# Kernel tuning notes

Hardware: AMD Instinct MI355X
Metric: run time of the kernel (lower is better)

Reference implementation:

```python
import jax, jax.numpy as jnp
import numpy as np

N, E = 50000, 800000          # nodes, edges
F_IN, H, C = 32, 64, 7        # input feats, hidden, classes
EPS = 1e-5                    # BatchNorm eps


def setup_inputs() -> dict:
    key = jax.random.key(0)
    ks = jax.random.split(key, 16)
    inp = {
        "x": jax.random.normal(ks[0], (N, F_IN), jnp.float32),
        "edge_index": jax.random.randint(ks[1], (2, E), 0, N),
        "edge_attr": jax.random.uniform(ks[2], (E, 1), jnp.float32),
    }

    def conv_params(k, cin, cout, i):
        k1, k2 = jax.random.split(k)
        s = 1.0 / np.sqrt(cin)
        inp[f"W{i}"] = jax.random.uniform(k1, (2, cin, cout), jnp.float32, -s, s)  # spline kernel weights
        inp[f"R{i}"] = jax.random.uniform(k2, (cin, cout), jnp.float32, -s, s)     # root weight
        inp[f"B{i}"] = jnp.zeros((cout,), jnp.float32)

    conv_params(ks[3], F_IN, H, 0)
    conv_params(ks[4], H, H, 1)
    conv_params(ks[5], H, C, 2)
    for i in range(2):  # BatchNorm (eval mode: running stats)
        inp[f"G{i}"] = jnp.ones((H,), jnp.float32)
        inp[f"BE{i}"] = jnp.zeros((H,), jnp.float32)
        inp[f"RM{i}"] = 0.1 * jax.random.normal(ks[6 + 2 * i], (H,), jnp.float32)
        inp[f"RV{i}"] = jax.random.uniform(ks[7 + 2 * i], (H,), jnp.float32, 0.5, 1.5)
    return inp


def spline_conv(x, src, dst, u, W, R, B):
    # dim=1, kernel_size=2, degree=1 open B-spline:
    # basis = (1-u, u) with weight indices (0, 1) for u in [0,1).
    basis = jnp.stack([1.0 - u, u], axis=1)               # [E, 2]
    msg = jnp.einsum('ec,ek,kco->eo', x[src], basis, W)    # gather + basis-weighted linear
    agg = jax.ops.segment_sum(msg, dst, num_segments=N)    # scatter-add
    deg = jax.ops.segment_sum(jnp.ones((src.shape[0],), x.dtype), dst, num_segments=N)
    agg = agg / jnp.maximum(deg, 1.0)[:, None]             # aggr='mean' (default)
    return agg + x @ R + B                                 # root weight + bias


def batch_norm(x, g, b, rm, rv):
    return (x - rm) * jax.lax.rsqrt(rv + EPS) * g + b


def reference(x, edge_index, edge_attr,
              W0, R0, B0, W1, R1, B1, W2, R2, B2,
              G0, BE0, RM0, RV0, G1, BE1, RM1, RV1):
    src, dst = edge_index[0], edge_index[1]
    u = edge_attr[:, 0]
    h = spline_conv(x, src, dst, u, W0, R0, B0)
    h = jax.nn.elu(batch_norm(h, G0, BE0, RM0, RV0))
    h = spline_conv(h, src, dst, u, W1, R1, B1)
    h = jax.nn.elu(batch_norm(h, G1, BE1, RM1, RV1))
    h = spline_conv(h, src, dst, u, W2, R2, B2)
    return jax.nn.log_softmax(h, axis=1)
```

## Files before the change

kernel.cpp:

```cpp
#include <hip/hip_runtime.h>
#include <hip/hip_fp16.h>
#include <math.h>

#define NN 50000
#define NE 800000
#define EPSV 1e-5f
#define BSHIFT 7
#define BSIZE 128
#define NB 391
#define CAP 3840

typedef _Float16 h2f   __attribute__((ext_vector_type(2)));
typedef _Float16 f16x8 __attribute__((ext_vector_type(8)));
typedef float    f32x4 __attribute__((ext_vector_type(4)));

__global__ __launch_bounds__(64) void prep_all_kernel(
        const float* __restrict__ W0, const float* __restrict__ R0,
        const float* __restrict__ W1, const float* __restrict__ R1,
        const float* __restrict__ W2, const float* __restrict__ R2,
        const float* __restrict__ B0, const float* __restrict__ B1,
        const float* __restrict__ G0, const float* __restrict__ BE0,
        const float* __restrict__ RM0, const float* __restrict__ RV0,
        const float* __restrict__ G1, const float* __restrict__ BE1,
        const float* __restrict__ RM1, const float* __restrict__ RV1,
        __half* __restrict__ Bf0, __half* __restrict__ Bf1, __half* __restrict__ Bf7,
        float* __restrict__ bn0, float* __restrict__ bn1,
        int* __restrict__ bcursor) {
    int lane = threadIdx.x;
    int bid = blockIdx.x;
    int c = lane & 15;
    int kbase = ((lane >> 4) << 3);
    _Float16 vals[8];
    if (bid < 12) {
        int ks = bid >> 2, nt = bid & 3;
        int n = nt * 16 + c;
#pragma unroll
        for (int j = 0; j < 8; ++j) {
            int kg = ks * 32 + kbase + j;
            float v = (kg < 64) ? W0[(kg & 1) * 2048 + (kg >> 1) * 64 + n]
                                : R0[(kg - 64) * 64 + n];
            vals[j] = (_Float16)v;
        }
        *reinterpret_cast<f16x8*>(Bf0 + ((size_t)(bid * 64 + lane)) * 8) =
            *reinterpret_cast<f16x8*>(vals);
    } else if (bid < 36) {
        int t = bid - 12;
        int ks = t >> 2, nt = t & 3;
        int n = nt * 16 + c;
#pragma unroll
        for (int j = 0; j < 8; ++j) {
            int kg = ks * 32 + kbase + j;
            float v = (kg < 128) ? W1[(kg & 1) * 4096 + (kg >> 1) * 64 + n]
                                 : R1[(kg - 128) * 64 + n];
            vals[j] = (_Float16)v;
        }
        *reinterpret_cast<f16x8*>(Bf1 + ((size_t)(t * 64 + lane)) * 8) =
            *reinterpret_cast<f16x8*>(vals);
    } else if (bid < 40) {
        int ksnt = bid - 36;
        int ks = ksnt >> 1, nt = ksnt & 1;
#pragma unroll
        for (int j = 0; j < 8; ++j) {
            int k = ks * 32 + kbase + j;
            float v = 0.f;
            if (nt == 0) {
                if (c < 7)                 v = W2[k * 7 + c];
                else if (c >= 8 && c < 15) v = W2[448 + k * 7 + (c - 8)];
            } else {
                if (c < 7)                 v = R2[k * 7 + c];
            }
            vals[j] = (_Float16)v;
        }
        *reinterpret_cast<f16x8*>(Bf7 + ((size_t)(ksnt * 64 + lane)) * 8) =
            *reinterpret_cast<f16x8*>(vals);
    } else if (bid == 40) {
        float s = G0[lane] * rsqrtf(RV0[lane] + EPSV);
        bn0[lane] = s;
        bn0[64 + lane] = B0[lane] * s + BE0[lane] - RM0[lane] * s;
    } else if (bid == 41) {
        float s = G1[lane] * rsqrtf(RV1[lane] + EPSV);
        bn1[lane] = s;
        bn1[64 + lane] = B1[lane] * s + BE1[lane] - RM1[lane] * s;
    } else {
        int b = (bid - 42) * 64 + lane;
        if (b < NB) bcursor[b] = b * CAP;
    }
}

__global__ __launch_bounds__(256) void binB_xh_kernel(
        const int* __restrict__ src, const int* __restrict__ dst,
        const float* __restrict__ attr, int* __restrict__ bcursor,
        unsigned* __restrict__ es1su, unsigned char* __restrict__ es1dl, int E,
        const float* __restrict__ x, __half* __restrict__ xh) {
    __shared__ int hist[NB];
    __shared__ int base[NB];
    if (blockIdx.x >= NB) {
        int t = (blockIdx.x - NB) * 256 + threadIdx.x;
        size_t idx = (size_t)t * 8;
        if (idx < (size_t)NN * 32) {
            float4 f0 = *reinterpret_cast<const float4*>(x + idx);
            float4 f1 = *reinterpret_cast<const float4*>(x + idx + 4);
            _Float16 v[8] = {(_Float16)f0.x, (_Float16)f0.y, (_Float16)f0.z, (_Float16)f0.w,
                             (_Float16)f1.x, (_Float16)f1.y, (_Float16)f1.z, (_Float16)f1.w};
            *reinterpret_cast<f16x8*>(xh + idx) = *reinterpret_cast<f16x8*>(v);
        }
        return;
    }
    for (int i = threadIdx.x; i < NB; i += blockDim.x) hist[i] = 0;
    __syncthreads();
    const int chunk = (E + NB - 1) / NB;
    int e0 = blockIdx.x * chunk;
    int e1 = e0 + chunk; if (e1 > E) e1 = E;
    unsigned su[8]; unsigned char dlv[8]; short bv[8];
#pragma unroll
    for (int j = 0; j < 8; ++j) {
        int e = e0 + threadIdx.x + j * 256;
        if (e < e1) {
            int d = dst[e];
            int b = d >> BSHIFT;
            __half uh = __float2half_rn(attr[e]);
            su[j]  = ((unsigned)src[e] << 16) | (unsigned)__half_as_ushort(uh);
            dlv[j] = (unsigned char)(d & (BSIZE - 1));
            bv[j]  = (short)b;
            atomicAdd(&hist[b], 1);
        }
    }
    __syncthreads();
    for (int i = threadIdx.x; i < NB; i += blockDim.x) {
        int cnt = hist[i];
        base[i] = cnt ? atomicAdd(&bcursor[i], cnt) : 0;
        hist[i] = 0;
    }
    __syncthreads();
#pragma unroll
    for (int j = 0; j < 8; ++j) {
        int e = e0 + threadIdx.x + j * 256;
        if (e < e1) {
            int b = bv[j];
            int slot = base[b] + atomicAdd(&hist[b], 1);
            es1su[slot] = su[j];
            es1dl[slot] = dlv[j];
        }
    }
}

__global__ __launch_bounds__(256) void placeC_kernel(const int* __restrict__ bcursor,
                                                     const unsigned* __restrict__ es1su,
                                                     const unsigned char* __restrict__ es1dl,
                                                     int2* __restrict__ rowrange,
                                                     uint2* __restrict__ es8) {
    __shared__ int hist[BSIZE];
    __shared__ int stmp[BSIZE];
    __shared__ int cur[BSIZE];
    int b = blockIdx.x;
    int t = threadIdx.x;
    int bs = b * CAP;
    int be = bcursor[b];
    if (t < BSIZE) hist[t] = 0;
    __syncthreads();
    unsigned su[10]; unsigned char dlv[10];
#pragma unroll
    for (int j = 0; j < 10; ++j) {
        int i = bs + t + j * 256;
        if (i < be) {
            su[j]  = es1su[i];
            dlv[j] = es1dl[i];
            atomicAdd(&hist[dlv[j]], 1);
        }
    }
    __syncthreads();
    if (t < BSIZE) {
        int v = hist[t];
        int pv = (v + 15) & ~15;
        int incl = pv;
#pragma unroll
        for (int o = 1; o < 64; o <<= 1) {
            int nv = __shfl_up(incl, o, 64);
            if ((t & 63) >= o) incl += nv;
        }
        stmp[t] = incl;
    }
    __syncthreads();
    if (t < BSIZE) {
        int v = hist[t];
        int pv = (v + 15) & ~15;
        int excl = stmp[t] - pv + ((t >= 64) ? stmp[63] : 0);
        cur[t] = excl;
        int node = b * BSIZE + t;
        if (node < NN) {
            int2 rr; rr.x = bs + excl; rr.y = (v << 16) | pv;
            rowrange[node] = rr;
        }
    }
    __syncthreads();
#pragma unroll
    for (int j = 0; j < 10; ++j) {
        int i = bs + t + j * 256;
        if (i < be) {
            unsigned r = su[j];
            int dl = dlv[j];
            int slot = bs + atomicAdd(&cur[dl], 1);
            __half uh = __ushort_as_half((unsigned short)(r & 0xffffu));
            __half2 p = __halves2half2(__hsub(__ushort_as_half((unsigned short)0x3C00u), uh), uh);
            uint2 rec;
            rec.x = r >> 16;
            rec.y = *reinterpret_cast<unsigned*>(&p);
            es8[slot] = rec;
        }
    }
    __syncthreads();
    if (t < BSIZE) {
        int v = hist[t];
        int pv = (v + 15) & ~15;
        int start = bs + cur[t];
        int endp  = bs + (cur[t] - v) + pv;
        uint2 z; z.x = 0u; z.y = 0u;
        for (int k = start; k < endp; ++k) es8[k] = z;
    }
}

__global__ __launch_bounds__(256, 8) void gatherS32_kernel(const int2* __restrict__ rowrange,
                                                           const uint2* __restrict__ es8,
                                                           const __half* __restrict__ xh,
                                                           __half* __restrict__ S, int n_nodes) {
    int n = (blockIdx.x * blockDim.x + threadIdx.x) >> 6;
    int lane = threadIdx.x & 63;
    if (n >= n_nodes) return;
    int2 rr = rowrange[n];
    int beg  = __builtin_amdgcn_readfirstlane(rr.x);
    int meta = __builtin_amdgcn_readfirstlane(rr.y);
    int end = beg + (meta & 0xffff);
    const unsigned c2 = (unsigned)((lane & 31) << 1);
    const char* xb = (const char*)xh;
    float a0 = 0.f, a1 = 0.f, a2 = 0.f, a3 = 0.f;
    float a4 = 0.f, a5 = 0.f, a6 = 0.f, a7 = 0.f;
    float b0 = 0.f, b1 = 0.f, b2 = 0.f, b3 = 0.f;
    float b4 = 0.f, b5 = 0.f, b6 = 0.f, b7 = 0.f;
    int i = beg + (lane >> 5);
    for (; i + 14 < end; i += 16) {
        uint2 q0 = es8[i];
        uint2 q1 = es8[i + 2];
        uint2 q2 = es8[i + 4];
        uint2 q3 = es8[i + 6];
        uint2 q4 = es8[i + 8];
        uint2 q5 = es8[i + 10];
        uint2 q6 = es8[i + 12];
        uint2 q7 = es8[i + 14];
        __half x0 = *(const __half*)(xb + ((q0.x << 6) | c2));
        __half x1 = *(const __half*)(xb + ((q1.x << 6) | c2));
        __half x2 = *(const __half*)(xb + ((q2.x << 6) | c2));
        __half x3 = *(const __half*)(xb + ((q3.x << 6) | c2));
        __half x4 = *(const __half*)(xb + ((q4.x << 6) | c2));
        __half x5 = *(const __half*)(xb + ((q5.x << 6) | c2));
        __half x6 = *(const __half*)(xb + ((q6.x << 6) | c2));
        __half x7 = *(const __half*)(xb + ((q7.x << 6) | c2));
        __half2 u0 = __builtin_bit_cast(__half2, q0.y);
        __half2 u1 = __builtin_bit_cast(__half2, q1.y);
        __half2 u2 = __builtin_bit_cast(__half2, q2.y);
        __half2 u3 = __builtin_bit_cast(__half2, q3.y);
        __half2 u4 = __builtin_bit_cast(__half2, q4.y);
        __half2 u5 = __builtin_bit_cast(__half2, q5.y);
        __half2 u6 = __builtin_bit_cast(__half2, q6.y);
        __half2 u7 = __builtin_bit_cast(__half2, q7.y);
        float f0 = __half2float(x0), f1 = __half2float(x1);
        float f2 = __half2float(x2), f3 = __half2float(x3);
        float f4 = __half2float(x4), f5 = __half2float(x5);
        float f6 = __half2float(x6), f7 = __half2float(x7);
        a0 = fmaf(__low2float(u0), f0, a0); b0 = fmaf(__high2float(u0), f0, b0);
        a1 = fmaf(__low2float(u1), f1, a1); b1 = fmaf(__high2float(u1), f1, b1);
        a2 = fmaf(__low2float(u2), f2, a2); b2 = fmaf(__high2float(u2), f2, b2);
        a3 = fmaf(__low2float(u3), f3, a3); b3 = fmaf(__high2float(u3), f3, b3);
        a4 = fmaf(__low2float(u4), f4, a4); b4 = fmaf(__high2float(u4), f4, b4);
        a5 = fmaf(__low2float(u5), f5, a5); b5 = fmaf(__high2float(u5), f5, b5);
        a6 = fmaf(__low2float(u6), f6, a6); b6 = fmaf(__high2float(u6), f6, b6);
        a7 = fmaf(__low2float(u7), f7, a7); b7 = fmaf(__high2float(u7), f7, b7);
    }
    float a = ((a0 + a1) + (a2 + a3)) + ((a4 + a5) + (a6 + a7));
    float b = ((b0 + b1) + (b2 + b3)) + ((b4 + b5) + (b6 + b7));
    a += __shfl_xor(a, 32);
    b += __shfl_xor(b, 32);
    float degv = (float)(meta >> 16);
    if (degv < 1.f) degv = 1.f;
    float inv = 1.f / degv;
    if (lane < 32) {
        reinterpret_cast<__half2*>(S + (size_t)n * 64)[lane & 31] = __floats2half2_rn(a * inv, b * inv);
    }
}

__global__ __launch_bounds__(256, 8) void gatherS64_kernel(const int2* __restrict__ rowrange,
                                                           const uint2* __restrict__ es8,
                                                           const __half* __restrict__ ht,
                                                           __half* __restrict__ S, int n_nodes) {
    int n = (blockIdx.x * blockDim.x + threadIdx.x) >> 6;
    int lane = threadIdx.x & 63;
    if (n >= n_nodes) return;
    int2 rr = rowrange[n];
    int beg  = __builtin_amdgcn_readfirstlane(rr.x);
    int meta = __builtin_amdgcn_readfirstlane(rr.y);
    int end = beg + (meta & 0xffff);
    const unsigned c2 = (unsigned)(lane << 1);
    const char* xb = (const char*)ht;
    float a0 = 0.f, a1 = 0.f, a2 = 0.f, a3 = 0.f;
    float b0 = 0.f, b1 = 0.f, b2 = 0.f, b3 = 0.f;
    for (int i = beg; i + 7 < end; i += 8) {
        uint4 p0 = *reinterpret_cast<const uint4*>(es8 + i);
        uint4 p1 = *reinterpret_cast<const uint4*>(es8 + i + 2);
        uint4 p2 = *reinterpret_cast<const uint4*>(es8 + i + 4);
        uint4 p3 = *reinterpret_cast<const uint4*>(es8 + i + 6);
        __half x0 = *(const __half*)(xb + ((p0.x << 7) | c2));
        __half x1 = *(const __half*)(xb + ((p0.z << 7) | c2));
        __half x2 = *(const __half*)(xb + ((p1.x << 7) | c2));
        __half x3 = *(const __half*)(xb + ((p1.z << 7) | c2));
        __half x4 = *(const __half*)(xb + ((p2.x << 7) | c2));
        __half x5 = *(const __half*)(xb + ((p2.z << 7) | c2));
        __half x6 = *(const __half*)(xb + ((p3.x << 7) | c2));
        __half x7 = *(const __half*)(xb + ((p3.z << 7) | c2));
        __half2 u0 = __builtin_bit_cast(__half2, p0.y);
        __half2 u1 = __builtin_bit_cast(__half2, p0.w);
        __half2 u2 = __builtin_bit_cast(__half2, p1.y);
        __half2 u3 = __builtin_bit_cast(__half2, p1.w);
        __half2 u4 = __builtin_bit_cast(__half2, p2.y);
        __half2 u5 = __builtin_bit_cast(__half2, p2.w);
        __half2 u6 = __builtin_bit_cast(__half2, p3.y);
        __half2 u7 = __builtin_bit_cast(__half2, p3.w);
        float f0 = __half2float(x0), f1 = __half2float(x1);
        float f2 = __half2float(x2), f3 = __half2float(x3);
        float f4 = __half2float(x4), f5 = __half2float(x5);
        float f6 = __half2float(x6), f7 = __half2float(x7);
        a0 = fmaf(__low2float(u0), f0, a0); b0 = fmaf(__high2float(u0), f0, b0);
        a1 = fmaf(__low2float(u1), f1, a1); b1 = fmaf(__high2float(u1), f1, b1);
        a2 = fmaf(__low2float(u2), f2, a2); b2 = fmaf(__high2float(u2), f2, b2);
        a3 = fmaf(__low2float(u3), f3, a3); b3 = fmaf(__high2float(u3), f3, b3);
        a0 = fmaf(__low2float(u4), f4, a0); b0 = fmaf(__high2float(u4), f4, b0);
        a1 = fmaf(__low2float(u5), f5, a1); b1 = fmaf(__high2float(u5), f5, b1);
        a2 = fmaf(__low2float(u6), f6, a2); b2 = fmaf(__high2float(u6), f6, b2);
        a3 = fmaf(__low2float(u7), f7, a3); b3 = fmaf(__high2float(u7), f7, b3);
    }
    float a = (a0 + a1) + (a2 + a3);
    float b = (b0 + b1) + (b2 + b3);
    float degv = (float)(meta >> 16);
    if (degv < 1.f) degv = 1.f;
    float inv = 1.f / degv;
    reinterpret_cast<__half2*>(S + (size_t)n * 128)[lane] = __floats2half2_rn(a * inv, b * inv);
}

__global__ __launch_bounds__(256) void gemmL0_kernel(const __half* __restrict__ S,
                                                     const __half* __restrict__ xh,
                                                     const __half* __restrict__ Bf0,
                                                     const float* __restrict__ bn,
                                                     __half* __restrict__ hout, int n_nodes) {
    const int lane = threadIdx.x & 63;
    const int wid  = threadIdx.x >> 6;
    int m0 = (blockIdx.x * 4 + wid) * 16;
    if (m0 >= n_nodes) return;
    f32x4 acc[4];
#pragma unroll
    for (int i = 0; i < 4; ++i) acc[i] = (f32x4){0.f, 0.f, 0.f, 0.f};
    const int arow = m0 + (lane & 15);
    const int koff = ((lane >> 4) << 3);
    const f16x8* bf = reinterpret_cast<const f16x8*>(Bf0);
    const _Float16* sp = (const _Float16*)S  + (size_t)arow * 64 + koff;
    const _Float16* xp = (const _Float16*)xh + (size_t)arow * 32 + koff;
    f16x8 a0 = *reinterpret_cast<const f16x8*>(sp);
    f16x8 a1 = *reinterpret_cast<const f16x8*>(sp + 32);
    f16x8 a2 = *reinterpret_cast<const f16x8*>(xp);
#pragma unroll
    for (int nt = 0; nt < 4; ++nt)
        acc[nt] = __builtin_amdgcn_mfma_f32_16x16x32_f16(a0, bf[nt * 64 + lane], acc[nt], 0, 0, 0);
#pragma unroll
    for (int nt = 0; nt < 4; ++nt)
        acc[nt] = __builtin_amdgcn_mfma_f32_16x16x32_f16(a1, bf[(4 + nt) * 64 + lane], acc[nt], 0, 0, 0);
#pragma unroll
    for (int nt = 0; nt < 4; ++nt)
        acc[nt] = __builtin_amdgcn_mfma_f32_16x16x32_f16(a2, bf[(8 + nt) * 64 + lane], acc[nt], 0, 0, 0);
    const int c_lo  = lane & 15;
    const int rbase = ((lane >> 4) << 2);
#pragma unroll
    for (int nt = 0; nt < 4; ++nt) {
        int cc = nt * 16 + c_lo;
        float sc = bn[cc], sh = bn[64 + cc];
#pragma unroll
        for (int r = 0; r < 4; ++r) {
            int row = m0 + rbase + r;
            if (row < n_nodes) {
                float v = acc[nt][r] * sc + sh;
                v = v > 0.f ? v : expm1f(v);
                hout[(size_t)row * 64 + cc] = __float2half(v);
            }
        }
    }
}

__global__ __launch_bounds__(256) void gemmL1_7_kernel(const __half* __restrict__ S,
                                                       const __half* __restrict__ hin,
                                                       const __half* __restrict__ Bf1,
                                                       const __half* __restrict__ Bf7,
                                                       const float* __restrict__ bn,
                                                       const float* __restrict__ Bb2,
                                                       __half* __restrict__ Yab7H,
                                                       float* __restrict__ Z7,
                                                       int n_nodes) {
    __shared__ __align__(16) char ldsH[64 * 128];
    const int lane = threadIdx.x & 63;
    const int wid  = threadIdx.x >> 6;
    int m0 = (blockIdx.x * 4 + wid) * 16;
    if (m0 >= n_nodes) return;
    f32x4 acc[4];
#pragma unroll
    for (int i = 0; i < 4; ++i) acc[i] = (f32x4){0.f, 0.f, 0.f, 0.f};
    const int arow = m0 + (lane & 15);
    const int g = lane >> 4;
    const int koff = g << 3;
    const f16x8* bf = reinterpret_cast<const f16x8*>(Bf1);
    const _Float16* sp = (const _Float16*)S   + (size_t)arow * 128 + koff;
    const _Float16* hp = (const _Float16*)hin + (size_t)arow * 64  + koff;
#pragma unroll
    for (int ks = 0; ks < 6; ++ks) {
        f16x8 av = (ks < 4) ? *reinterpret_cast<const f16x8*>(sp + ks * 32)
                            : *reinterpret_cast<const f16x8*>(hp + (ks - 4) * 32);
#pragma unroll
        for (int nt = 0; nt < 4; ++nt)
            acc[nt] = __builtin_amdgcn_mfma_f32_16x16x32_f16(av, bf[(ks * 4 + nt) * 64 + lane], acc[nt], 0, 0, 0);
    }
    const int c_lo  = lane & 15;
    const int rbase = ((lane >> 4) << 2);
#pragma unroll
    for (int nt = 0; nt < 4; ++nt) {
        int cc = nt * 16 + c_lo;
        float sc = bn[cc], sh = bn[64 + cc];
#pragma unroll
        for (int r = 0; r < 4; ++r) {
            float v = acc[nt][r] * sc + sh;
            v = v > 0.f ? v : expm1f(v);
            int rl = wid * 16 + rbase + r;
            *reinterpret_cast<__half*>(ldsH + ((rl * 128 + cc * 2) ^ ((rl & 7) << 4))) = __float2half(v);
        }
    }

    const int rowl = wid * 16 + (lane & 15);
    const int swz = (rowl & 7) << 4;
    f32x4 acc7[2];
    acc7[0] = (f32x4){0.f, 0.f, 0.f, 0.f};
    acc7[1] = (f32x4){0.f, 0.f, 0.f, 0.f};
    const f16x8* bf7 = reinterpret_cast<const f16x8*>(Bf7);
#pragma unroll
    for (int ks = 0; ks < 2; ++ks) {
        f16x8 av = *reinterpret_cast<const f16x8*>(ldsH + ((rowl * 128 + ks * 64 + g * 16) ^ swz));
#pragma unroll
        for (int nt = 0; nt < 2; ++nt)
            acc7[nt] = __builtin_amdgcn_mfma_f32_16x16x32_f16(av, bf7[(ks * 2 + nt) * 64 + lane], acc7[nt], 0, 0, 0);
    }
#pragma unroll
    for (int r = 0; r < 4; ++r) {
        int row = m0 + rbase + r;
        if (row < n_nodes) {
            if (c_lo < 7) {
                Yab7H[((size_t)row << 4) + 2 * c_lo] = __float2half(acc7[0][r]);
                Z7[((size_t)row << 3) + c_lo] = acc7[1][r] + Bb2[c_lo];
            } else if (c_lo >= 8 && c_lo < 15) {
                Yab7H[((size_t)row << 4) + 2 * (c_lo - 8) + 1] = __float2half(acc7[0][r]);
            }
        }
    }
}

__global__ void gather7_final_kernel(const int2* __restrict__ rowrange,
                                     const uint2* __restrict__ es8,
                                     const __half2* __restrict__ Yab7H,
                                     const float* __restrict__ Z7,
                                     float* __restrict__ out, int n_nodes) {
    int t = blockIdx.x * blockDim.x + threadIdx.x;
    int n = t >> 3;
    int c = t & 7;
    if (n >= n_nodes) return;
    int2 rr = rowrange[n];
    int beg = rr.x;
    int end = beg + (rr.y & 0xffff);
    const unsigned c4 = (unsigned)(c << 2);
    const char* yb = (const char*)Yab7H;
    float acc0 = 0.f, acc1 = 0.f, acc2 = 0.f, acc3 = 0.f;
    if (c < 7) {
        for (int i = beg; i + 7 < end; i += 8) {
            uint2 q0 = es8[i];
            uint2 q1 = es8[i + 1];
            uint2 q2 = es8[i + 2];
            uint2 q3 = es8[i + 3];
            uint2 q4 = es8[i + 4];
            uint2 q5 = es8[i + 5];
            uint2 q6 = es8[i + 6];
            uint2 q7 = es8[i + 7];
            __half2 v0 = *(const __half2*)(yb + ((q0.x << 5) | c4));
            __half2 v1 = *(const __half2*)(yb + ((q1.x << 5) | c4));
            __half2 v2 = *(const __half2*)(yb + ((q2.x << 5) | c4));
            __half2 v3 = *(const __half2*)(yb + ((q3.x << 5) | c4));
            __half2 v4 = *(const __half2*)(yb + ((q4.x << 5) | c4));
            __half2 v5 = *(const __half2*)(yb + ((q5.x << 5) | c4));
            __half2 v6 = *(const __half2*)(yb + ((q6.x << 5) | c4));
            __half2 v7 = *(const __half2*)(yb + ((q7.x << 5) | c4));
            acc0 = __builtin_amdgcn_fdot2(__builtin_bit_cast(h2f, v0), __builtin_bit_cast(h2f, q0.y), acc0, false);
            acc1 = __builtin_amdgcn_fdot2(__builtin_bit_cast(h2f, v1), __builtin_bit_cast(h2f, q1.y), acc1, false);
            acc2 = __builtin_amdgcn_fdot2(__builtin_bit_cast(h2f, v2), __builtin_bit_cast(h2f, q2.y), acc2, false);
            acc3 = __builtin_amdgcn_fdot2(__builtin_bit_cast(h2f, v3), __builtin_bit_cast(h2f, q3.y), acc3, false);
            acc0 = __builtin_amdgcn_fdot2(__builtin_bit_cast(h2f, v4), __builtin_bit_cast(h2f, q4.y), acc0, false);
            acc1 = __builtin_amdgcn_fdot2(__builtin_bit_cast(h2f, v5), __builtin_bit_cast(h2f, q5.y), acc1, false);
            acc2 = __builtin_amdgcn_fdot2(__builtin_bit_cast(h2f, v6), __builtin_bit_cast(h2f, q6.y), acc2, false);
            acc3 = __builtin_amdgcn_fdot2(__builtin_bit_cast(h2f, v7), __builtin_bit_cast(h2f, q7.y), acc3, false);
        }
    }
    float acc = (acc0 + acc1) + (acc2 + acc3);
    float degv = (float)(rr.y >> 16);
    if (degv < 1.f) degv = 1.f;
    float v = (c < 7) ? (acc / degv + Z7[(n << 3) + c]) : -1e30f;
    float m = v;
#pragma unroll
    for (int o = 1; o < 8; o <<= 1) m = fmaxf(m, __shfl_xor(m, o, 8));
    float ex = (c < 7) ? expf(v - m) : 0.f;
    float ssum = ex;
#pragma unroll
    for (int o = 1; o < 8; o <<= 1) ssum += __shfl_xor(ssum, o, 8);
    if (c < 7) out[n * 7 + c] = v - m - logf(ssum);
}

extern "C" void kernel_launch(void* const* d_in, const int* in_sizes, int n_in,
                              void* d_out, int out_size, void* d_ws, size_t ws_size,
                              hipStream_t stream) {
    const float* x    = (const float*)d_in[0];
    const int*   ei   = (const int*)d_in[1];
    const float* attr = (const float*)d_in[2];
    const float* W0 = (const float*)d_in[3];
    const float* R0 = (const float*)d_in[4];
    const float* B0 = (const float*)d_in[5];
    const float* W1 = (const float*)d_in[6];
    const float* R1 = (const float*)d_in[7];
    const float* B1 = (const float*)d_in[8];
    const float* W2 = (const float*)d_in[9];
    const float* R2 = (const float*)d_in[10];
    const float* B2 = (const float*)d_in[11];
    const float* G0  = (const float*)d_in[12];
    const float* BE0 = (const float*)d_in[13];
    const float* RM0 = (const float*)d_in[14];
    const float* RV0 = (const float*)d_in[15];
    const float* G1  = (const float*)d_in[16];
    const float* BE1 = (const float*)d_in[17];
    const float* RM1 = (const float*)d_in[18];
    const float* RV1 = (const float*)d_in[19];

    const int* src = ei;
    const int* dst = ei + NE;
    float* out = (float*)d_out;

    char* ws = (char*)d_ws;
    size_t off = 0;
    auto alloc = [&](size_t bytes) { char* p = ws + off; off += (bytes + 255) & ~size_t(255); return p; };
    int*           bcursor  = (int*)          alloc(NB * sizeof(int));
    int2*          rowrange = (int2*)         alloc((size_t)NN * sizeof(int2));
    unsigned*      es1su    = (unsigned*)     alloc((size_t)NB * CAP * sizeof(unsigned));
    unsigned char* es1dl    = (unsigned char*)alloc((size_t)NB * CAP * sizeof(unsigned char));
    uint2*         es8      = (uint2*)        alloc((size_t)NB * CAP * sizeof(uint2));
    __half*        Bf0      = (__half*)       alloc((size_t)12 * 64 * 8 * sizeof(__half));
    __half*        Bf1      = (__half*)       alloc((size_t)24 * 64 * 8 * sizeof(__half));
    __half*        Bf7      = (__half*)       alloc((size_t)4 * 64 * 8 * sizeof(__half));
    float*         bn0      = (float*)        alloc(128 * sizeof(float));
    float*         bn1      = (float*)        alloc(128 * sizeof(float));
    __half*        xh       = (__half*)       alloc((size_t)(NN + 64) * 32 * sizeof(__half));
    __half*        S        = (__half*)       alloc((size_t)(NN + 64) * 128 * sizeof(__half));
    __half*        h0       = (__half*)       alloc((size_t)(NN + 64) * 64 * sizeof(__half));
    __half*        Yab7H    = (__half*)       alloc((size_t)NN * 16 * sizeof(__half));
    float*         Z7       = (float*)        alloc((size_t)NN * 8 * sizeof(float));

    const int B = 256;
    const int gM    = ((NN + 15) / 16 + 3) / 4;
    const int gGath = (NN * 64) / B;
    const int gN8   = (NN * 8 + B - 1) / B;
    const int gConv = ((NN * 32 / 8) + B - 1) / B;
    const int gPrep = 42 + (NB + 63) / 64;

    prep_all_kernel<<<gPrep, 64, 0, stream>>>(W0, R0, W1, R1, W2, R2, B0, B1,
                                              G0, BE0, RM0, RV0, G1, BE1, RM1, RV1,
                                              Bf0, Bf1, Bf7, bn0, bn1, bcursor);

    binB_xh_kernel<<<NB + gConv, B, 0, stream>>>(src, dst, attr, bcursor, es1su, es1dl, NE, x, xh);

    placeC_kernel<<<NB, B, 0, stream>>>(bcursor, es1su, es1dl, rowrange, es8);

    gatherS32_kernel<<<gGath, B, 0, stream>>>(rowrange, es8, xh, S, NN);
    gemmL0_kernel<<<gM, B, 0, stream>>>(S, xh, Bf0, bn0, h0, NN);

    gatherS64_kernel<<<gGath, B, 0, stream>>>(rowrange, es8, h0, S, NN);
    gemmL1_7_kernel<<<gM, B, 0, stream>>>(S, h0, Bf1, Bf7, bn1, B2, Yab7H, Z7, NN);

    gather7_final_kernel<<<gN8, B, 0, stream>>>(rowrange, es8, (const __half2*)Yab7H, Z7, out, NN);
}
```

Before: 209.8 us.

## Fuse neighbor gather with MFMA GEMM per layer via LDS staging

Merges each gather kernel with the following GEMM kernel: a block of four waves gathers 16 node rows into swizzled LDS, then wave 0 runs the MFMA GEMM with BN/ELU epilogue. This removes the global S intermediate (write and re-read) and two kernel launches. In exchange only one of four waves does the GEMM after a block barrier, and each wave now processes four nodes serially, which may reduce gather parallelism and latency hiding.

```diff
diff --git a/kernel.cpp b/kernel.cpp
--- a/kernel.cpp
+++ b/kernel.cpp
@@ -219,160 +219,106 @@
     }
 }
 
-__global__ __launch_bounds__(256, 8) void gatherS32_kernel(const int2* __restrict__ rowrange,
-                                                           const uint2* __restrict__ es8,
-                                                           const __half* __restrict__ xh,
-                                                           __half* __restrict__ S, int n_nodes) {
-    int n = (blockIdx.x * blockDim.x + threadIdx.x) >> 6;
-    int lane = threadIdx.x & 63;
-    if (n >= n_nodes) return;
-    int2 rr = rowrange[n];
-    int beg  = __builtin_amdgcn_readfirstlane(rr.x);
-    int meta = __builtin_amdgcn_readfirstlane(rr.y);
-    int end = beg + (meta & 0xffff);
-    const unsigned c2 = (unsigned)((lane & 31) << 1);
-    const char* xb = (const char*)xh;
-    float a0 = 0.f, a1 = 0.f, a2 = 0.f, a3 = 0.f;
-    float a4 = 0.f, a5 = 0.f, a6 = 0.f, a7 = 0.f;
-    float b0 = 0.f, b1 = 0.f, b2 = 0.f, b3 = 0.f;
-    float b4 = 0.f, b5 = 0.f, b6 = 0.f, b7 = 0.f;
-    int i = beg + (lane >> 5);
-    for (; i + 14 < end; i += 16) {
-        uint2 q0 = es8[i];
-        uint2 q1 = es8[i + 2];
-        uint2 q2 = es8[i + 4];
-        uint2 q3 = es8[i + 6];
-        uint2 q4 = es8[i + 8];
-        uint2 q5 = es8[i + 10];
-        uint2 q6 = es8[i + 12];
-        uint2 q7 = es8[i + 14];
-        __half x0 = *(const __half*)(xb + ((q0.x << 6) | c2));
-        __half x1 = *(const __half*)(xb + ((q1.x << 6) | c2));
-        __half x2 = *(const __half*)(xb + ((q2.x << 6) | c2));
-        __half x3 = *(const __half*)(xb + ((q3.x << 6) | c2));
-        __half x4 = *(const __half*)(xb + ((q4.x << 6) | c2));
-        __half x5 = *(const __half*)(xb + ((q5.x << 6) | c2));
-        __half x6 = *(const __half*)(xb + ((q6.x << 6) | c2));
-        __half x7 = *(const __half*)(xb + ((q7.x << 6) | c2));
-        __half2 u0 = __builtin_bit_cast(__half2, q0.y);
-        __half2 u1 = __builtin_bit_cast(__half2, q1.y);
-        __half2 u2 = __builtin_bit_cast(__half2, q2.y);
-        __half2 u3 = __builtin_bit_cast(__half2, q3.y);
-        __half2 u4 = __builtin_bit_cast(__half2, q4.y);
-        __half2 u5 = __builtin_bit_cast(__half2, q5.y);
-        __half2 u6 = __builtin_bit_cast(__half2, q6.y);
-        __half2 u7 = __builtin_bit_cast(__half2, q7.y);
-        float f0 = __half2float(x0), f1 = __half2float(x1);
-        float f2 = __half2float(x2), f3 = __half2float(x3);
-        float f4 = __half2float(x4), f5 = __half2float(x5);
-        float f6 = __half2float(x6), f7 = __half2float(x7);
-        a0 = fmaf(__low2float(u0), f0, a0); b0 = fmaf(__high2float(u0), f0, b0);
-        a1 = fmaf(__low2float(u1), f1, a1); b1 = fmaf(__high2float(u1), f1, b1);
-        a2 = fmaf(__low2float(u2), f2, a2); b2 = fmaf(__high2float(u2), f2, b2);
-        a3 = fmaf(__low2float(u3), f3, a3); b3 = fmaf(__high2float(u3), f3, b3);
-        a4 = fmaf(__low2float(u4), f4, a4); b4 = fmaf(__high2float(u4), f4, b4);
-        a5 = fmaf(__low2float(u5), f5, a5); b5 = fmaf(__high2float(u5), f5, b5);
-        a6 = fmaf(__low2float(u6), f6, a6); b6 = fmaf(__high2float(u6), f6, b6);
-        a7 = fmaf(__low2float(u7), f7, a7); b7 = fmaf(__high2float(u7), f7, b7);
-    }
-    float a = ((a0 + a1) + (a2 + a3)) + ((a4 + a5) + (a6 + a7));
-    float b = ((b0 + b1) + (b2 + b3)) + ((b4 + b5) + (b6 + b7));
-    a += __shfl_xor(a, 32);
-    b += __shfl_xor(b, 32);
-    float degv = (float)(meta >> 16);
-    if (degv < 1.f) degv = 1.f;
-    float inv = 1.f / degv;
-    if (lane < 32) {
-        reinterpret_cast<__half2*>(S + (size_t)n * 64)[lane & 31] = __floats2half2_rn(a * inv, b * inv);
-    }
-}
-
-__global__ __launch_bounds__(256, 8) void gatherS64_kernel(const int2* __restrict__ rowrange,
-                                                           const uint2* __restrict__ es8,
-                                                           const __half* __restrict__ ht,
-                                                           __half* __restrict__ S, int n_nodes) {
-    int n = (blockIdx.x * blockDim.x + threadIdx.x) >> 6;
-    int lane = threadIdx.x & 63;
-    if (n >= n_nodes) return;
-    int2 rr = rowrange[n];
-    int beg  = __builtin_amdgcn_readfirstlane(rr.x);
-    int meta = __builtin_amdgcn_readfirstlane(rr.y);
-    int end = beg + (meta & 0xffff);
-    const unsigned c2 = (unsigned)(lane << 1);
-    const char* xb = (const char*)ht;
-    float a0 = 0.f, a1 = 0.f, a2 = 0.f, a3 = 0.f;
-    float b0 = 0.f, b1 = 0.f, b2 = 0.f, b3 = 0.f;
-    for (int i = beg; i + 7 < end; i += 8) {
-        uint4 p0 = *reinterpret_cast<const uint4*>(es8 + i);
-        uint4 p1 = *reinterpret_cast<const uint4*>(es8 + i + 2);
-        uint4 p2 = *reinterpret_cast<const uint4*>(es8 + i + 4);
-        uint4 p3 = *reinterpret_cast<const uint4*>(es8 + i + 6);
-        __half x0 = *(const __half*)(xb + ((p0.x << 7) | c2));
-        __half x1 = *(const __half*)(xb + ((p0.z << 7) | c2));
-        __half x2 = *(const __half*)(xb + ((p1.x << 7) | c2));
-        __half x3 = *(const __half*)(xb + ((p1.z << 7) | c2));
-        __half x4 = *(const __half*)(xb + ((p2.x << 7) | c2));
-        __half x5 = *(const __half*)(xb + ((p2.z << 7) | c2));
-        __half x6 = *(const __half*)(xb + ((p3.x << 7) | c2));
-        __half x7 = *(const __half*)(xb + ((p3.z << 7) | c2));
-        __half2 u0 = __builtin_bit_cast(__half2, p0.y);
-        __half2 u1 = __builtin_bit_cast(__half2, p0.w);
-        __half2 u2 = __builtin_bit_cast(__half2, p1.y);
-        __half2 u3 = __builtin_bit_cast(__half2, p1.w);
-        __half2 u4 = __builtin_bit_cast(__half2, p2.y);
-        __half2 u5 = __builtin_bit_cast(__half2, p2.w);
-        __half2 u6 = __builtin_bit_cast(__half2, p3.y);
-        __half2 u7 = __builtin_bit_cast(__half2, p3.w);
-        float f0 = __half2float(x0), f1 = __half2float(x1);
-        float f2 = __half2float(x2), f3 = __half2float(x3);
-        float f4 = __half2float(x4), f5 = __half2float(x5);
-        float f6 = __half2float(x6), f7 = __half2float(x7);
-        a0 = fmaf(__low2float(u0), f0, a0); b0 = fmaf(__high2float(u0), f0, b0);
-        a1 = fmaf(__low2float(u1), f1, a1); b1 = fmaf(__high2float(u1), f1, b1);
-        a2 = fmaf(__low2float(u2), f2, a2); b2 = fmaf(__high2float(u2), f2, b2);
-        a3 = fmaf(__low2float(u3), f3, a3); b3 = fmaf(__high2float(u3), f3, b3);
-        a0 = fmaf(__low2float(u4), f4, a0); b0 = fmaf(__high2float(u4), f4, b0);
-        a1 = fmaf(__low2float(u5), f5, a1); b1 = fmaf(__high2float(u5), f5, b1);
-        a2 = fmaf(__low2float(u6), f6, a2); b2 = fmaf(__high2float(u6), f6, b2);
-        a3 = fmaf(__low2float(u7), f7, a3); b3 = fmaf(__high2float(u7), f7, b3);
-    }
-    float a = (a0 + a1) + (a2 + a3);
-    float b = (b0 + b1) + (b2 + b3);
-    float degv = (float)(meta >> 16);
-    if (degv < 1.f) degv = 1.f;
-    float inv = 1.f / degv;
-    reinterpret_cast<__half2*>(S + (size_t)n * 128)[lane] = __floats2half2_rn(a * inv, b * inv);
-}
-
-__global__ __launch_bounds__(256) void gemmL0_kernel(const __half* __restrict__ S,
+__global__ __launch_bounds__(256, 8) void gf0_kernel(const int2* __restrict__ rowrange,
+                                                     const uint2* __restrict__ es8,
                                                      const __half* __restrict__ xh,
                                                      const __half* __restrict__ Bf0,
                                                      const float* __restrict__ bn,
-                                                     __half* __restrict__ hout, int n_nodes) {
+                                                     __half* __restrict__ h0, int n_nodes) {
+    __shared__ __align__(16) char ldsS[16 * 128];
     const int lane = threadIdx.x & 63;
     const int wid  = threadIdx.x >> 6;
-    int m0 = (blockIdx.x * 4 + wid) * 16;
-    if (m0 >= n_nodes) return;
+    const int nb = blockIdx.x * 16;
+    const unsigned c2 = (unsigned)((lane & 31) << 1);
+    const char* xb = (const char*)xh;
+#pragma unroll 1
+    for (int k = 0; k < 4; ++k) {
+        int row = wid * 4 + k;
+        int n = nb + row;
+        if (n >= n_nodes) break;
+        int2 rr = rowrange[n];
+        int beg  = __builtin_amdgcn_readfirstlane(rr.x);
+        int meta = __builtin_amdgcn_readfirstlane(rr.y);
+        int end = beg + (meta & 0xffff);
+        float a0 = 0.f, a1 = 0.f, a2 = 0.f, a3 = 0.f;
+        float a4 = 0.f, a5 = 0.f, a6 = 0.f, a7 = 0.f;
+        float b0 = 0.f, b1 = 0.f, b2 = 0.f, b3 = 0.f;
+        float b4 = 0.f, b5 = 0.f, b6 = 0.f, b7 = 0.f;
+        int i = beg + (lane >> 5);
+        for (; i + 14 < end; i += 16) {
+            uint2 q0 = es8[i];
+            uint2 q1 = es8[i + 2];
+            uint2 q2 = es8[i + 4];
+            uint2 q3 = es8[i + 6];
+            uint2 q4 = es8[i + 8];
+            uint2 q5 = es8[i + 10];
+            uint2 q6 = es8[i + 12];
+            uint2 q7 = es8[i + 14];
+            __half x0 = *(const __half*)(xb + ((q0.x << 6) | c2));
+            __half x1 = *(const __half*)(xb + ((q1.x << 6) | c2));
+            __half x2 = *(const __half*)(xb + ((q2.x << 6) | c2));
+            __half x3 = *(const __half*)(xb + ((q3.x << 6) | c2));
+            __half x4 = *(const __half*)(xb + ((q4.x << 6) | c2));
+            __half x5 = *(const __half*)(xb + ((q5.x << 6) | c2));
+            __half x6 = *(const __half*)(xb + ((q6.x << 6) | c2));
+            __half x7 = *(const __half*)(xb + ((q7.x << 6) | c2));
+            __half2 u0 = __builtin_bit_cast(__half2, q0.y);
+            __half2 u1 = __builtin_bit_cast(__half2, q1.y);
+            __half2 u2 = __builtin_bit_cast(__half2, q2.y);
+            __half2 u3 = __builtin_bit_cast(__half2, q3.y);
+            __half2 u4 = __builtin_bit_cast(__half2, q4.y);
+            __half2 u5 = __builtin_bit_cast(__half2, q5.y);
+            __half2 u6 = __builtin_bit_cast(__half2, q6.y);
+            __half2 u7 = __builtin_bit_cast(__half2, q7.y);
+            float f0 = __half2float(x0), f1 = __half2float(x1);
+            float f2 = __half2float(x2), f3 = __half2float(x3);
+            float f4 = __half2float(x4), f5 = __half2float(x5);
+            float f6 = __half2float(x6), f7 = __half2float(x7);
+            a0 = fmaf(__low2float(u0), f0, a0); b0 = fmaf(__high2float(u0), f0, b0);
+            a1 = fmaf(__low2float(u1), f1, a1); b1 = fmaf(__high2float(u1), f1, b1);
+            a2 = fmaf(__low2float(u2), f2, a2); b2 = fmaf(__high2float(u2), f2, b2);
+            a3 = fmaf(__low2float(u3), f3, a3); b3 = fmaf(__high2float(u3), f3, b3);
+            a4 = fmaf(__low2float(u4), f4, a4); b4 = fmaf(__high2float(u4), f4, b4);
+            a5 = fmaf(__low2float(u5), f5, a5); b5 = fmaf(__high2float(u5), f5, b5);
+            a6 = fmaf(__low2float(u6), f6, a6); b6 = fmaf(__high2float(u6), f6, b6);
+            a7 = fmaf(__low2float(u7), f7, a7); b7 = fmaf(__high2float(u7), f7, b7);
+        }
+        float a = ((a0 + a1) + (a2 + a3)) + ((a4 + a5) + (a6 + a7));
+        float b = ((b0 + b1) + (b2 + b3)) + ((b4 + b5) + (b6 + b7));
+        a += __shfl_xor(a, 32);
+        b += __shfl_xor(b, 32);
+        float degv = (float)(meta >> 16);
+        if (degv < 1.f) degv = 1.f;
+        float inv = 1.f / degv;
+        if (lane < 32) {
+            int byte = (row * 128 + (lane & 31) * 4) ^ ((row & 7) << 4);
+            *reinterpret_cast<__half2*>(ldsS + byte) = __floats2half2_rn(a * inv, b * inv);
+        }
+    }
+    __syncthreads();
+    if (wid != 0) return;
+
+    const int m0 = nb;
     f32x4 acc[4];
 #pragma unroll
     for (int i = 0; i < 4; ++i) acc[i] = (f32x4){0.f, 0.f, 0.f, 0.f};
-    const int arow = m0 + (lane & 15);
-    const int koff = ((lane >> 4) << 3);
+    const int rowl = lane & 15;
+    const int g = lane >> 4;
+    const int koff = g << 3;
+    const int swz = (rowl & 7) << 4;
     const f16x8* bf = reinterpret_cast<const f16x8*>(Bf0);
-    const _Float16* sp = (const _Float16*)S  + (size_t)arow * 64 + koff;
-    const _Float16* xp = (const _Float16*)xh + (size_t)arow * 32 + koff;
-    f16x8 a0 = *reinterpret_cast<const f16x8*>(sp);
-    f16x8 a1 = *reinterpret_cast<const f16x8*>(sp + 32);
-    f16x8 a2 = *reinterpret_cast<const f16x8*>(xp);
+    f16x8 a0v = *reinterpret_cast<const f16x8*>(ldsS + ((rowl * 128 + g * 16) ^ swz));
+    f16x8 a1v = *reinterpret_cast<const f16x8*>(ldsS + ((rowl * 128 + 64 + g * 16) ^ swz));
+    f16x8 a2v = *reinterpret_cast<const f16x8*>((const _Float16*)xh + (size_t)(m0 + rowl) * 32 + koff);
 #pragma unroll
     for (int nt = 0; nt < 4; ++nt)
-        acc[nt] = __builtin_amdgcn_mfma_f32_16x16x32_f16(a0, bf[nt * 64 + lane], acc[nt], 0, 0, 0);
+        acc[nt] = __builtin_amdgcn_mfma_f32_16x16x32_f16(a0v, bf[nt * 64 + lane], acc[nt], 0, 0, 0);
 #pragma unroll
     for (int nt = 0; nt < 4; ++nt)
-        acc[nt] = __builtin_amdgcn_mfma_f32_16x16x32_f16(a1, bf[(4 + nt) * 64 + lane], acc[nt], 0, 0, 0);
+        acc[nt] = __builtin_amdgcn_mfma_f32_16x16x32_f16(a1v, bf[(4 + nt) * 64 + lane], acc[nt], 0, 0, 0);
 #pragma unroll
     for (int nt = 0; nt < 4; ++nt)
-        acc[nt] = __builtin_amdgcn_mfma_f32_16x16x32_f16(a2, bf[(8 + nt) * 64 + lane], acc[nt], 0, 0, 0);
+        acc[nt] = __builtin_amdgcn_mfma_f32_16x16x32_f16(a2v, bf[(8 + nt) * 64 + lane], acc[nt], 0, 0, 0);
     const int c_lo  = lane & 15;
     const int rbase = ((lane >> 4) << 2);
 #pragma unroll
@@ -381,43 +327,104 @@
         float sc = bn[cc], sh = bn[64 + cc];
 #pragma unroll
         for (int r = 0; r < 4; ++r) {
-            int row = m0 + rbase + r;
-            if (row < n_nodes) {
+            int rw = m0 + rbase + r;
+            if (rw < n_nodes) {
                 float v = acc[nt][r] * sc + sh;
                 v = v > 0.f ? v : expm1f(v);
-                hout[(size_t)row * 64 + cc] = __float2half(v);
+                h0[(size_t)rw * 64 + cc] = __float2half(v);
             }
         }
     }
 }
 
-__global__ __launch_bounds__(256) void gemmL1_7_kernel(const __half* __restrict__ S,
-                                                       const __half* __restrict__ hin,
-                                                       const __half* __restrict__ Bf1,
-                                                       const __half* __restrict__ Bf7,
-                                                       const float* __restrict__ bn,
-                                                       const float* __restrict__ Bb2,
-                                                       __half* __restrict__ Yab7H,
-                                                       float* __restrict__ Z7,
-                                                       int n_nodes) {
-    __shared__ __align__(16) char ldsH[64 * 128];
+__global__ __launch_bounds__(256, 8) void gf1_kernel(const int2* __restrict__ rowrange,
+                                                     const uint2* __restrict__ es8,
+                                                     const __half* __restrict__ h0,
+                                                     const __half* __restrict__ Bf1,
+                                                     const __half* __restrict__ Bf7,
+                                                     const float* __restrict__ bn,
+                                                     const float* __restrict__ Bb2,
+                                                     __half* __restrict__ Yab7H,
+                                                     float* __restrict__ Z7,
+                                                     int n_nodes) {
+    __shared__ __align__(16) char ldsS[16 * 256];
+    __shared__ __align__(16) char ldsH[16 * 128];
     const int lane = threadIdx.x & 63;
     const int wid  = threadIdx.x >> 6;
-    int m0 = (blockIdx.x * 4 + wid) * 16;
-    if (m0 >= n_nodes) return;
+    const int nb = blockIdx.x * 16;
+    const unsigned c2 = (unsigned)(lane << 1);
+    const char* xb = (const char*)h0;
+#pragma unroll 1
+    for (int k = 0; k < 4; ++k) {
+        int row = wid * 4 + k;
+        int n = nb + row;
+        if (n >= n_nodes) break;
+        int2 rr = rowrange[n];
+        int beg  = __builtin_amdgcn_readfirstlane(rr.x);
+        int meta = __builtin_amdgcn_readfirstlane(rr.y);
+        int end = beg + (meta & 0xffff);
+        float a0 = 0.f, a1 = 0.f, a2 = 0.f, a3 = 0.f;
+        float b0 = 0.f, b1 = 0.f, b2 = 0.f, b3 = 0.f;
+        for (int i = beg; i + 7 < end; i += 8) {
+            uint4 p0 = *reinterpret_cast<const uint4*>(es8 + i);
+            uint4 p1 = *reinterpret_cast<const uint4*>(es8 + i + 2);
+            uint4 p2 = *reinterpret_cast<const uint4*>(es8 + i + 4);
+            uint4 p3 = *reinterpret_cast<const uint4*>(es8 + i + 6);
+            __half x0 = *(const __half*)(xb + ((p0.x << 7) | c2));
+            __half x1 = *(const __half*)(xb + ((p0.z << 7) | c2));
+            __half x2 = *(const __half*)(xb + ((p1.x << 7) | c2));
+            __half x3 = *(const __half*)(xb + ((p1.z << 7) | c2));
+            __half x4 = *(const __half*)(xb + ((p2.x << 7) | c2));
+            __half x5 = *(const __half*)(xb + ((p2.z << 7) | c2));
+            __half x6 = *(const __half*)(xb + ((p3.x << 7) | c2));
+            __half x7 = *(const __half*)(xb + ((p3.z << 7) | c2));
+            __half2 u0 = __builtin_bit_cast(__half2, p0.y);
+            __half2 u1 = __builtin_bit_cast(__half2, p0.w);
+            __half2 u2 = __builtin_bit_cast(__half2, p1.y);
+            __half2 u3 = __builtin_bit_cast(__half2, p1.w);
+            __half2 u4 = __builtin_bit_cast(__half2, p2.y);
+            __half2 u5 = __builtin_bit_cast(__half2, p2.w);
+            __half2 u6 = __builtin_bit_cast(__half2, p3.y);
+            __half2 u7 = __builtin_bit_cast(__half2, p3.w);
+            float f0 = __half2float(x0), f1 = __half2float(x1);
+            float f2 = __half2float(x2), f3 = __half2float(x3);
+            float f4 = __half2float(x4), f5 = __half2float(x5);
+            float f6 = __half2float(x6), f7 = __half2float(x7);
+            a0 = fmaf(__low2float(u0), f0, a0); b0 = fmaf(__high2float(u0), f0, b0);
+            a1 = fmaf(__low2float(u1), f1, a1); b1 = fmaf(__high2float(u1), f1, b1);
+            a2 = fmaf(__low2float(u2), f2, a2); b2 = fmaf(__high2float(u2), f2, b2);
+            a3 = fmaf(__low2float(u3), f3, a3); b3 = fmaf(__high2float(u3), f3, b3);
+            a0 = fmaf(__low2float(u4), f4, a0); b0 = fmaf(__high2float(u4), f4, b0);
+            a1 = fmaf(__low2float(u5), f5, a1); b1 = fmaf(__high2float(u5), f5, b1);
+            a2 = fmaf(__low2float(u6), f6, a2); b2 = fmaf(__high2float(u6), f6, b2);
+            a3 = fmaf(__low2float(u7), f7, a3); b3 = fmaf(__high2float(u7), f7, b3);
+        }
+        float a = (a0 + a1) + (a2 + a3);
+        float b = (b0 + b1) + (b2 + b3);
+        float degv = (float)(meta >> 16);
+        if (degv < 1.f) degv = 1.f;
+        float inv = 1.f / degv;
+        int byte = (row * 256 + lane * 4) ^ ((row & 7) << 4);
+        *reinterpret_cast<__half2*>(ldsS + byte) = __floats2half2_rn(a * inv, b * inv);
+    }
+    __syncthreads();
+    if (wid != 0) return;
+
+    const int m0 = nb;
     f32x4 acc[4];
 #pragma unroll
     for (int i = 0; i < 4; ++i) acc[i] = (f32x4){0.f, 0.f, 0.f, 0.f};
-    const int arow = m0 + (lane & 15);
+    const int rowl = lane & 15;
     const int g = lane >> 4;
     const int koff = g << 3;
+    const int swz = (rowl & 7) << 4;
     const f16x8* bf = reinterpret_cast<const f16x8*>(Bf1);
-    const _Float16* sp = (const _Float16*)S   + (size_t)arow * 128 + koff;
-    const _Float16* hp = (const _Float16*)hin + (size_t)arow * 64  + koff;
+    const _Float16* hp = (const _Float16*)h0 + (size_t)(m0 + rowl) * 64 + koff;
 #pragma unroll
     for (int ks = 0; ks < 6; ++ks) {
-        f16x8 av = (ks < 4) ? *reinterpret_cast<const f16x8*>(sp + ks * 32)
-                            : *reinterpret_cast<const f16x8*>(hp + (ks - 4) * 32);
+        f16x8 av;
+        if (ks < 4) av = *reinterpret_cast<const f16x8*>(ldsS + ((rowl * 256 + ks * 64 + g * 16) ^ swz));
+        else        av = *reinterpret_cast<const f16x8*>(hp + (ks - 4) * 32);
 #pragma unroll
         for (int nt = 0; nt < 4; ++nt)
             acc[nt] = __builtin_amdgcn_mfma_f32_16x16x32_f16(av, bf[(ks * 4 + nt) * 64 + lane], acc[nt], 0, 0, 0);
@@ -432,13 +439,11 @@
         for (int r = 0; r < 4; ++r) {
             float v = acc[nt][r] * sc + sh;
             v = v > 0.f ? v : expm1f(v);
-            int rl = wid * 16 + rbase + r;
+            int rl = rbase + r;
             *reinterpret_cast<__half*>(ldsH + ((rl * 128 + cc * 2) ^ ((rl & 7) << 4))) = __float2half(v);
         }
     }
 
-    const int rowl = wid * 16 + (lane & 15);
-    const int swz = (rowl & 7) << 4;
     f32x4 acc7[2];
     acc7[0] = (f32x4){0.f, 0.f, 0.f, 0.f};
     acc7[1] = (f32x4){0.f, 0.f, 0.f, 0.f};
@@ -452,13 +457,13 @@
     }
 #pragma unroll
     for (int r = 0; r < 4; ++r) {
-        int row = m0 + rbase + r;
-        if (row < n_nodes) {
+        int rw = m0 + rbase + r;
+        if (rw < n_nodes) {
             if (c_lo < 7) {
-                Yab7H[((size_t)row << 4) + 2 * c_lo] = __float2half(acc7[0][r]);
-                Z7[((size_t)row << 3) + c_lo] = acc7[1][r] + Bb2[c_lo];
+                Yab7H[((size_t)rw << 4) + 2 * c_lo] = __float2half(acc7[0][r]);
+                Z7[((size_t)rw << 3) + c_lo] = acc7[1][r] + Bb2[c_lo];
             } else if (c_lo >= 8 && c_lo < 15) {
-                Yab7H[((size_t)row << 4) + 2 * (c_lo - 8) + 1] = __float2half(acc7[0][r]);
+                Yab7H[((size_t)rw << 4) + 2 * (c_lo - 8) + 1] = __float2half(acc7[0][r]);
             }
         }
     }
@@ -563,14 +568,12 @@
     float*         bn0      = (float*)        alloc(128 * sizeof(float));
     float*         bn1      = (float*)        alloc(128 * sizeof(float));
     __half*        xh       = (__half*)       alloc((size_t)(NN + 64) * 32 * sizeof(__half));
-    __half*        S        = (__half*)       alloc((size_t)(NN + 64) * 128 * sizeof(__half));
     __half*        h0       = (__half*)       alloc((size_t)(NN + 64) * 64 * sizeof(__half));
     __half*        Yab7H    = (__half*)       alloc((size_t)NN * 16 * sizeof(__half));
     float*         Z7       = (float*)        alloc((size_t)NN * 8 * sizeof(float));
 
     const int B = 256;
-    const int gM    = ((NN + 15) / 16 + 3) / 4;
-    const int gGath = (NN * 64) / B;
+    const int gF    = (NN + 15) / 16;
     const int gN8   = (NN * 8 + B - 1) / B;
     const int gConv = ((NN * 32 / 8) + B - 1) / B;
     const int gPrep = 42 + (NB + 63) / 64;
@@ -583,11 +586,9 @@
 
     placeC_kernel<<<NB, B, 0, stream>>>(bcursor, es1su, es1dl, rowrange, es8);
 
-    gatherS32_kernel<<<gGath, B, 0, stream>>>(rowrange, es8, xh, S, NN);
-    gemmL0_kernel<<<gM, B, 0, stream>>>(S, xh, Bf0, bn0, h0, NN);
-
-    gatherS64_kernel<<<gGath, B, 0, stream>>>(rowrange, es8, h0, S, NN);
-    gemmL1_7_kernel<<<gM, B, 0, stream>>>(S, h0, Bf1, Bf7, bn1, B2, Yab7H, Z7, NN);
+    gf0_kernel<<<gF, B, 0, stream>>>(rowrange, es8, xh, Bf0, bn0, h0, NN);
+
+    gf1_kernel<<<gF, B, 0, stream>>>(rowrange, es8, h0, Bf1, Bf7, bn1, B2, Yab7H, Z7, NN);
 
     gather7_final_kernel<<<gN8, B, 0, stream>>>(rowrange, es8, (const __half2*)Yab7H, Z7, out, NN);
 }
```

New measurement: 202.3 us. -3.6%, faster.
